# Performance work log

Hardware: AMD Instinct MI355X
Metric: run time of the kernel (lower is better)

The kernel has to match this reference:

```python
import jax, jax.numpy as jnp
import numpy as np
from jax.ops import segment_sum, segment_max

N_NODES = 100000
N_EDGES = 1600000
IN, HID, OUT = 256, 64, 40
NEG_SLOPE = 0.2  # DGL GATConv default


def setup_inputs() -> dict:
    key = jax.random.key(0)
    ks = jax.random.split(key, 12)
    feat = jax.random.normal(ks[0], (N_NODES, IN), dtype=jnp.float32)
    src = jax.random.randint(ks[1], (N_EDGES,), 0, N_NODES)
    dst = jax.random.randint(ks[2], (N_EDGES,), 0, N_NODES)
    def xavier(k, shape):
        fan = sum(shape)
        return jax.random.normal(k, shape, dtype=jnp.float32) * jnp.sqrt(2.0 / fan)
    return {
        "feat": feat, "src": src, "dst": dst,
        "W1": xavier(ks[3], (IN, HID)),  "b1": jnp.zeros((HID,), jnp.float32),
        "al1": xavier(ks[4], (HID,)),    "ar1": xavier(ks[5], (HID,)),
        "W2": xavier(ks[6], (HID, OUT)), "b2": jnp.zeros((OUT,), jnp.float32),
        "al2": xavier(ks[7], (OUT,)),    "ar2": xavier(ks[8], (OUT,)),
    }


def gat_layer(x, W, b, attn_l, attn_r, src, dst, n):
    # z: [N, F_out] projected features
    z = x @ W
    el = z @ attn_l          # [N] source attention logits
    er = z @ attn_r          # [N] destination attention logits
    e = jax.nn.leaky_relu(el[src] + er[dst], NEG_SLOPE)  # [E]
    # segment (per-destination) softmax over incoming edges
    m = segment_max(e, dst, num_segments=n)              # [N]
    w = jnp.exp(e - m[dst])                              # [E]
    s = segment_sum(w, dst, num_segments=n)              # [N]
    alpha = w / s[dst]                                   # [E]
    # scatter-add aggregation of alpha * z[src]
    out = segment_sum(alpha[:, None] * z[src], dst, num_segments=n)
    return out + b


def reference(feat, src, dst, W1, b1, al1, ar1, W2, b2, al2, ar2):
    n = feat.shape[0]
    h = gat_layer(feat, W1, b1, al1, ar1, src, dst, n)
    h = jax.nn.relu(h)  # dropout is identity in eval mode
    h = gat_layer(h, W2, b2, al2, ar2, src, dst, n)
    return jax.nn.log_softmax(h, axis=-1)  # [N, out_size]
```

## Files before the change

### kernel.cpp

```cpp
#include <hip/hip_runtime.h>
#include <math.h>

constexpr int NN   = 100000;
constexpr int NE   = 1600000;
constexpr int FIN  = 256;
constexpr int HID  = 64;
constexpr int FOUT = 40;
constexpr float SLOPE = 0.2f;
constexpr int NBUCK = (NN + 127) / 128;
constexpr int TILE_A = 2048;
constexpr int NWG_A = (NE + TILE_A - 1) / TILE_A;
constexpr int NT_GEMM = (NN + 63) / 64;
constexpr int HB = 64;
constexpr int HIST_EPB = 4096;
constexpr int NWG_H = (NE + HIST_EPB - 1) / HIST_EPB;

typedef short  short8  __attribute__((ext_vector_type(8)));
typedef float  floatx4 __attribute__((ext_vector_type(4)));

__device__ inline unsigned short f2bf(float x) {
    union { float f; unsigned int u; } c; c.f = x;
    unsigned int u = c.u;
    return (unsigned short)((u + 0x7FFF + ((u >> 16) & 1)) >> 16);
}

__device__ inline float readlane_f(float v, int l) {
    return __int_as_float(__builtin_amdgcn_readlane(__float_as_int(v), l));
}

__device__ inline void scan_buckets(const int* __restrict__ gcnt,
                                    int* __restrict__ bofs,
                                    int* __restrict__ tsum, int t)
{
    int i0 = 4 * t;
    int c0 = (i0 + 0 < NBUCK) ? gcnt[i0 + 0] : 0;
    int c1 = (i0 + 1 < NBUCK) ? gcnt[i0 + 1] : 0;
    int c2 = (i0 + 2 < NBUCK) ? gcnt[i0 + 2] : 0;
    int c3 = (i0 + 3 < NBUCK) ? gcnt[i0 + 3] : 0;
    int s = c0 + c1 + c2 + c3;
    tsum[t] = s;
    __syncthreads();
    for (int off = 1; off < 256; off <<= 1) {
        int x = (t >= off) ? tsum[t - off] : 0;
        __syncthreads();
        tsum[t] += x;
        __syncthreads();
    }
    int e0 = tsum[t] - s;
    if (i0 + 0 <= NBUCK) bofs[i0 + 0] = e0;
    if (i0 + 1 <= NBUCK) bofs[i0 + 1] = e0 + c0;
    if (i0 + 2 <= NBUCK) bofs[i0 + 2] = e0 + c0 + c1;
    if (i0 + 3 <= NBUCK) bofs[i0 + 3] = e0 + c0 + c1 + c2;
    __syncthreads();
}

__global__ __launch_bounds__(256) void prep_kernel(
    const float* __restrict__ W1, unsigned short* __restrict__ W1T,
    const float* __restrict__ W2, const float* __restrict__ al2,
    const float* __restrict__ ar2,
    float* __restrict__ wl2, float* __restrict__ wr2,
    const int* __restrict__ dst, int* __restrict__ bcnt)
{
    const int t = threadIdx.x;
    if (blockIdx.x < HB) {
        int idx = blockIdx.x * 256 + t;
        if (idx < FIN * HID) {
            int k = idx >> 6, n = idx & 63;
            W1T[n * FIN + k] = f2bf(W1[idx]);
        }
        if (blockIdx.x == 0 && t < HID) {
            int k = t;
            float a = 0.f, b = 0.f;
            #pragma unroll 8
            for (int j = 0; j < FOUT; ++j) {
                float wv = W2[k * FOUT + j];
                a += wv * al2[j]; b += wv * ar2[j];
            }
            wl2[k] = a; wr2[k] = b;
        }
    } else {
        __shared__ int hist[NBUCK];
        for (int i = t; i < NBUCK; i += 256) hist[i] = 0;
        __syncthreads();
        int base = (blockIdx.x - HB) * HIST_EPB + t * 16;
        #pragma unroll
        for (int k = 0; k < 4; ++k) {
            int idx = base + 4 * k;
            if (idx < NE) {
                const int4 d4 = *(const int4*)&dst[idx];
                atomicAdd(&hist[d4.x >> 7], 1); atomicAdd(&hist[d4.y >> 7], 1);
                atomicAdd(&hist[d4.z >> 7], 1); atomicAdd(&hist[d4.w >> 7], 1);
            }
        }
        __syncthreads();
        for (int i = t; i < NBUCK; i += 256) {
            int hv = hist[i];
            if (hv) atomicAdd(&bcnt[i], hv);
        }
    }
}

__global__ __launch_bounds__(256) void mega_kernel(
    const float* __restrict__ feat, const unsigned short* __restrict__ W1T,
    const float* __restrict__ al, const float* __restrict__ ar,
    const int* __restrict__ src, const int* __restrict__ dst,
    const int* __restrict__ bcnt, int* __restrict__ cur0,
    int* __restrict__ ebuck,
    _Float16* __restrict__ z, float* __restrict__ el, float* __restrict__ er)
{
    __shared__ int smem4[2 * NBUCK + 1 + 256];
    const int t = threadIdx.x;

    if (blockIdx.x < NT_GEMM) {
        const int ntile = blockIdx.x * 64;

        const int w  = t >> 6;
        const int l  = t & 63;
        const int lr = l & 15;
        const int q  = l >> 4;
        const int m0 = 16 * w;

        int n = ntile + m0 + lr; if (n >= NN) n = NN - 1;
        const float* __restrict__ arow = feat + (size_t)n * FIN;

        floatx4 acc[4];
        #pragma unroll
        for (int tile = 0; tile < 4; ++tile) acc[tile] = 0.f;

        #pragma unroll
        for (int kc = 0; kc < 8; ++kc) {
            const int koff = kc * 32 + 8 * q;
            const float4 fa = *(const float4*)(arow + koff);
            const float4 fb = *(const float4*)(arow + koff + 4);
            short8 av;
            av[0] = (short)f2bf(fa.x); av[1] = (short)f2bf(fa.y);
            av[2] = (short)f2bf(fa.z); av[3] = (short)f2bf(fa.w);
            av[4] = (short)f2bf(fb.x); av[5] = (short)f2bf(fb.y);
            av[6] = (short)f2bf(fb.z); av[7] = (short)f2bf(fb.w);
            #pragma unroll
            for (int tile = 0; tile < 4; ++tile) {
                const short8 bv = *(const short8*)(W1T + (16 * tile + lr) * FIN + koff);
                acc[tile] = __builtin_amdgcn_mfma_f32_16x16x32_bf16(av, bv, acc[tile], 0, 0, 0);
            }
        }

        float aln[4], arn[4];
        #pragma unroll
        for (int tile = 0; tile < 4; ++tile) {
            aln[tile] = al[16 * tile + lr];
            arn[tile] = ar[16 * tile + lr];
        }
        #pragma unroll
        for (int r = 0; r < 4; ++r) {
            int mg = ntile + m0 + 4 * q + r;
            float pl = 0.f, pr = 0.f;
            #pragma unroll
            for (int tile = 0; tile < 4; ++tile) {
                float zv = acc[tile][r];
                pl += zv * aln[tile]; pr += zv * arn[tile];
            }
            #pragma unroll
            for (int off = 8; off >= 1; off >>= 1) {
                pl += __shfl_xor(pl, off);
                pr += __shfl_xor(pr, off);
            }
            if (mg < NN) {
                #pragma unroll
                for (int tile = 0; tile < 4; ++tile)
                    z[(size_t)mg * HID + 16 * tile + lr] = (_Float16)acc[tile][r];
                if (lr == 0) { el[mg] = pl; er[mg] = pr; }
            }
        }
    } else {
        int* hist = smem4;
        int* bofs = smem4 + NBUCK;
        int* tsum = smem4 + 2 * NBUCK + 1;
        const int blk = blockIdx.x - NT_GEMM;
        const int e0 = blk * TILE_A;
        const int e1 = (e0 + TILE_A < NE) ? e0 + TILE_A : NE;

        for (int i = t; i < NBUCK; i += 256) hist[i] = 0;
        scan_buckets(bcnt, bofs, tsum, t);
        for (int e = e0 + t; e < e1; e += 256)
            atomicAdd(&hist[dst[e] >> 7], 1);
        __syncthreads();
        for (int i = t; i < NBUCK; i += 256) {
            int hv = hist[i];
            hist[i] = hv ? (bofs[i] + atomicAdd(&cur0[i], hv)) : 0;
        }
        __syncthreads();
        for (int e = e0 + t; e < e1; e += 256) {
            int d = dst[e], s_ = src[e];
            int p = atomicAdd(&hist[d >> 7], 1);
            ebuck[p] = (s_ << 7) | (d & 127);
        }
    }
}

__global__ __launch_bounds__(256) void partB_kernel(
    const int* __restrict__ bcnt, const int* __restrict__ ebuck,
    int* __restrict__ row_ptr, int* __restrict__ esrc)
{
    __shared__ int bofs[NBUCK + 1];
    __shared__ int tsum[256];
    __shared__ int sdeg[128];
    __shared__ int sscan[128];
    __shared__ int scur[128];
    const int b = blockIdx.x;
    const int n0 = b << 7;
    const int t = threadIdx.x;

    if (t < 128) sdeg[t] = 0;
    scan_buckets(bcnt, bofs, tsum, t);
    const int r0 = bofs[b], r1 = bofs[b + 1];

    for (int e = r0 + t; e < r1; e += 256)
        atomicAdd(&sdeg[ebuck[e] & 127], 1);
    __syncthreads();

    if (t < 128) sscan[t] = sdeg[t];
    __syncthreads();
    for (int off = 1; off < 128; off <<= 1) {
        int x = (t < 128 && t >= off) ? sscan[t - off] : 0;
        __syncthreads();
        if (t < 128) sscan[t] += x;
        __syncthreads();
    }
    if (t < 128) {
        int excl = sscan[t] - sdeg[t];
        if (n0 + t < NN) row_ptr[n0 + t] = r0 + excl;
        scur[t] = r0 + excl;
    }
    if (b == NBUCK - 1 && t == 0) row_ptr[NN] = NE;
    __syncthreads();

    for (int e = r0 + t; e < r1; e += 256) {
        int pk = ebuck[e];
        int p = atomicAdd(&scur[pk & 127], 1);
        esrc[p] = pk >> 7;
    }
}

template<bool FIRST>
__global__ __launch_bounds__(256) void gat_gather_kernel(
    const int* __restrict__ row_ptr, const int* __restrict__ esrc,
    const float* __restrict__ el, const float* __restrict__ er,
    const _Float16* __restrict__ zin, const float* __restrict__ b1,
    const float* __restrict__ wl2, const float* __restrict__ wr2,
    _Float16* __restrict__ hout, _Float16* __restrict__ haggout,
    float* __restrict__ el2, float* __restrict__ er2)
{
    const int w = threadIdx.x >> 6, lane = threadIdx.x & 63;
    const int d = blockIdx.x * 4 + w;
    const int r0 = row_ptr[d], r1 = row_ptr[d + 1];
    const int cnt = r1 - r0;
    const float erd = er[d];

    float accv = 0.f;
    float s = 0.f;

    if (cnt <= 64) {
        int sn = 0; float v = -INFINITY;
        if (lane < cnt) {
            sn = esrc[r0 + lane];
            v = el[sn] + erd;
            v = (v >= 0.f) ? v : SLOPE * v;
        }
        float m = v;
        #pragma unroll
        for (int off = 32; off >= 1; off >>= 1) m = fmaxf(m, __shfl_xor(m, off));
        float wv = (lane < cnt) ? __expf(v - m) : 0.f;
        s = wv;
        #pragma unroll
        for (int off = 32; off >= 1; off >>= 1) s += __shfl_xor(s, off);
        {
            int j = 0;
            for (; j + 8 <= cnt; j += 8) {
                float a0 = 0.f, a1 = 0.f;
                #pragma unroll
                for (int qq = 0; qq < 8; qq += 2) {
                    float w0 = readlane_f(wv, j + qq);
                    int   s0 = __builtin_amdgcn_readlane(sn, j + qq);
                    float w1 = readlane_f(wv, j + qq + 1);
                    int   s1 = __builtin_amdgcn_readlane(sn, j + qq + 1);
                    a0 += w0 * (float)zin[(size_t)s0 * HID + lane];
                    a1 += w1 * (float)zin[(size_t)s1 * HID + lane];
                }
                accv += a0 + a1;
            }
            for (; j < cnt; ++j) {
                float w0 = readlane_f(wv, j);
                int   s0 = __builtin_amdgcn_readlane(sn, j);
                accv += w0 * (float)zin[(size_t)s0 * HID + lane];
            }
        }
    } else {
        float m = -INFINITY;
        for (int e = r0 + lane; e < r1; e += 64) {
            float v = el[esrc[e]] + erd;
            v = (v >= 0.f) ? v : SLOPE * v;
            m = fmaxf(m, v);
        }
        #pragma unroll
        for (int off = 32; off >= 1; off >>= 1) m = fmaxf(m, __shfl_xor(m, off));
        for (int base = r0; base < r1; base += 64) {
            int e = base + lane;
            float wv = 0.f; int sn = 0;
            if (e < r1) {
                sn = esrc[e];
                float v = el[sn] + erd;
                v = (v >= 0.f) ? v : SLOPE * v;
                wv = __expf(v - m);
            }
            s += wv;
            int c = r1 - base; if (c > 64) c = 64;
            {
                int j = 0;
                for (; j + 4 <= c; j += 4) {
                    float a0 = 0.f, a1 = 0.f;
                    #pragma unroll
                    for (int qq = 0; qq < 4; qq += 2) {
                        float w0 = readlane_f(wv, j + qq);
                        int   s0 = __builtin_amdgcn_readlane(sn, j + qq);
                        float w1 = readlane_f(wv, j + qq + 1);
                        int   s1 = __builtin_amdgcn_readlane(sn, j + qq + 1);
                        a0 += w0 * (float)zin[(size_t)s0 * HID + lane];
                        a1 += w1 * (float)zin[(size_t)s1 * HID + lane];
                    }
                    accv += a0 + a1;
                }
                for (; j < c; ++j) {
                    float w0 = readlane_f(wv, j);
                    int   s0 = __builtin_amdgcn_readlane(sn, j);
                    accv += w0 * (float)zin[(size_t)s0 * HID + lane];
                }
            }
        }
        #pragma unroll
        for (int off = 32; off >= 1; off >>= 1) s += __shfl_xor(s, off);
    }

    float res = (cnt > 0) ? (accv / s) : 0.f;

    if (FIRST) {
        float hval = res + b1[lane];
        hval = (hval > 0.f) ? hval : 0.f;
        hout[(size_t)d * HID + lane] = (_Float16)hval;
        float pl = hval * wl2[lane];
        float pr = hval * wr2[lane];
        #pragma unroll
        for (int off = 32; off >= 1; off >>= 1) {
            pl += __shfl_xor(pl, off); pr += __shfl_xor(pr, off);
        }
        if (lane == 0) { el2[d] = pl; er2[d] = pr; }
    } else {
        haggout[(size_t)d * HID + lane] = (_Float16)res;
    }
}

__global__ __launch_bounds__(256) void out_kernel(
    const _Float16* __restrict__ hagg, const float* __restrict__ W2,
    const float* __restrict__ b2, float* __restrict__ out)
{
    __shared__ float sh[4][64];
    const int w = threadIdx.x >> 6, lane = threadIdx.x & 63;
    const int n = blockIdx.x * 4 + w;
    sh[w][lane] = (float)hagg[(size_t)n * HID + lane];
    __syncthreads();
    float acc = 0.f;
    if (lane < FOUT) {
        #pragma unroll 8
        for (int k = 0; k < HID; ++k) acc += sh[w][k] * W2[k * FOUT + lane];
    }
    float v = (lane < FOUT) ? acc + b2[lane] : -INFINITY;
    float mx = v;
    #pragma unroll
    for (int off = 32; off >= 1; off >>= 1) mx = fmaxf(mx, __shfl_xor(mx, off));
    float ex = (lane < FOUT) ? __expf(v - mx) : 0.f;
    float sm = ex;
    #pragma unroll
    for (int off = 32; off >= 1; off >>= 1) sm += __shfl_xor(sm, off);
    if (lane < FOUT) out[(size_t)n * FOUT + lane] = v - mx - __logf(sm);
}

extern "C" void kernel_launch(void* const* d_in, const int* in_sizes, int n_in,
                              void* d_out, int out_size, void* d_ws, size_t ws_size,
                              hipStream_t stream) {
    const float* feat = (const float*)d_in[0];
    const int*   src  = (const int*)d_in[1];
    const int*   dst  = (const int*)d_in[2];
    const float* W1   = (const float*)d_in[3];
    const float* b1   = (const float*)d_in[4];
    const float* al1  = (const float*)d_in[5];
    const float* ar1  = (const float*)d_in[6];
    const float* W2   = (const float*)d_in[7];
    const float* b2   = (const float*)d_in[8];
    const float* al2  = (const float*)d_in[9];
    const float* ar2  = (const float*)d_in[10];
    float* out = (float*)d_out;

    char* p = (char*)d_ws;
    _Float16* hagg = (_Float16*)p;
    _Float16* z1   = (_Float16*)p;  p += (size_t)NN * HID * 2;
    _Float16* h    = (_Float16*)p;  p += (size_t)NN * HID * 2;
    float* el1   = (float*)p;     p += (size_t)NN * 4;
    float* er1   = (float*)p;     p += (size_t)NN * 4;
    float* el2   = (float*)p;     p += (size_t)NN * 4;
    float* er2   = (float*)p;     p += (size_t)NN * 4;
    float* wl2   = (float*)p;     p += HID * 4;
    float* wr2   = (float*)p;     p += HID * 4;
    int*   bcnt  = (int*)p;       p += NBUCK * 4;
    int*   cur0  = (int*)p;       p += NBUCK * 4;
    int*   rowp  = (int*)p;       p += (NN + 1) * 4;
    int*   esrc  = (int*)p;       p += (size_t)NE * 4;
    int*   ebuck = (int*)p;       p += (size_t)NE * 4;
    unsigned short* w1t = (unsigned short*)p;

    hipMemsetAsync(bcnt, 0, 2 * NBUCK * sizeof(int), stream);

    prep_kernel<<<HB + NWG_H, 256, 0, stream>>>(
        W1, w1t, W2, al2, ar2, wl2, wr2, dst, bcnt);

    mega_kernel<<<NT_GEMM + NWG_A, 256, 0, stream>>>(
        feat, w1t, al1, ar1, src, dst, bcnt, cur0, ebuck, z1, el1, er1);

    partB_kernel<<<NBUCK, 256, 0, stream>>>(bcnt, ebuck, rowp, esrc);

    gat_gather_kernel<true><<<NN / 4, 256, 0, stream>>>(
        rowp, esrc, el1, er1, z1, b1, wl2, wr2, h, nullptr, el2, er2);

    gat_gather_kernel<false><<<NN / 4, 256, 0, stream>>>(
        rowp, esrc, el2, er2, h, nullptr, nullptr, nullptr,
        nullptr, hagg, nullptr, nullptr);

    out_kernel<<<NN / 4, 256, 0, stream>>>(hagg, W2, b2, out);
}
```

Measured before the change: 435.0 us.

## Fuse pipeline into two cooperative persistent kernels with grid syncs

Replaces the six kernel launches (prep, mega, partB, two gathers, output) with two cooperative persistent kernels. Stages are separated by grid-wide syncs and driven by grid-stride loops. The GEMM stage now stages the transposed bf16 W1 in LDS and takes a fixed 3/4 of the blocks, with the rest doing edge bucketing. The aim is to cut launch and tail overheads between stages, at the cost of grid-sync latency and occupancy-limited grid sizes for the gather phases.

```diff
diff --git a/kernel.cpp b/kernel.cpp
--- a/kernel.cpp
+++ b/kernel.cpp
@@ -1,5 +1,8 @@
 #include <hip/hip_runtime.h>
+#include <hip/hip_cooperative_groups.h>
 #include <math.h>
+
+namespace cg = cooperative_groups;
 
 constexpr int NN   = 100000;
 constexpr int NE   = 1600000;
@@ -9,11 +12,11 @@
 constexpr float SLOPE = 0.2f;
 constexpr int NBUCK = (NN + 127) / 128;
 constexpr int TILE_A = 2048;
-constexpr int NWG_A = (NE + TILE_A - 1) / TILE_A;
+constexpr int PA_CHUNKS = (NE + TILE_A - 1) / TILE_A;
 constexpr int NT_GEMM = (NN + 63) / 64;
-constexpr int HB = 64;
+constexpr int AK = 264;
 constexpr int HIST_EPB = 4096;
-constexpr int NWG_H = (NE + HIST_EPB - 1) / HIST_EPB;
+constexpr int NH = (NE + HIST_EPB - 1) / HIST_EPB;
 
 typedef short  short8  __attribute__((ext_vector_type(8)));
 typedef float  floatx4 __attribute__((ext_vector_type(4)));
@@ -54,65 +57,70 @@
     __syncthreads();
 }
 
-__global__ __launch_bounds__(256) void prep_kernel(
-    const float* __restrict__ W1, unsigned short* __restrict__ W1T,
+__global__ __launch_bounds__(256) void coopA(
+    const float* __restrict__ feat, const float* __restrict__ W1,
+    unsigned short* __restrict__ W1T,
     const float* __restrict__ W2, const float* __restrict__ al2,
     const float* __restrict__ ar2,
     float* __restrict__ wl2, float* __restrict__ wr2,
-    const int* __restrict__ dst, int* __restrict__ bcnt)
+    const int* __restrict__ src, const int* __restrict__ dst,
+    int* __restrict__ bcnt, int* __restrict__ cur0, int* __restrict__ ebuck,
+    const float* __restrict__ al, const float* __restrict__ ar,
+    _Float16* __restrict__ z, float* __restrict__ el, float* __restrict__ er,
+    int* __restrict__ row_ptr, int* __restrict__ esrc)
 {
-    const int t = threadIdx.x;
-    if (blockIdx.x < HB) {
-        int idx = blockIdx.x * 256 + t;
-        if (idx < FIN * HID) {
-            int k = idx >> 6, n = idx & 63;
-            W1T[n * FIN + k] = f2bf(W1[idx]);
-        }
-        if (blockIdx.x == 0 && t < HID) {
-            int k = t;
-            float a = 0.f, b = 0.f;
-            #pragma unroll 8
-            for (int j = 0; j < FOUT; ++j) {
-                float wv = W2[k * FOUT + j];
-                a += wv * al2[j]; b += wv * ar2[j];
-            }
-            wl2[k] = a; wr2[k] = b;
-        }
-    } else {
-        __shared__ int hist[NBUCK];
+    cg::grid_group gridg = cg::this_grid();
+    __shared__ int smem[8448];
+    const int t   = threadIdx.x;
+    const int bid = blockIdx.x;
+    const int G   = gridDim.x;
+
+    for (int idx = bid * 256 + t; idx < FIN * HID; idx += G * 256) {
+        int k = idx >> 6, n = idx & 63;
+        W1T[n * FIN + k] = f2bf(W1[idx]);
+    }
+    if (bid == 0 && t < HID) {
+        float a = 0.f, b = 0.f;
+        #pragma unroll 8
+        for (int j = 0; j < FOUT; ++j) {
+            float wv = W2[t * FOUT + j];
+            a += wv * al2[j]; b += wv * ar2[j];
+        }
+        wl2[t] = a; wr2[t] = b;
+    }
+    for (int hb = bid; hb < NH; hb += G) {
+        int* hist = smem;
         for (int i = t; i < NBUCK; i += 256) hist[i] = 0;
         __syncthreads();
-        int base = (blockIdx.x - HB) * HIST_EPB + t * 16;
-        #pragma unroll
-        for (int k = 0; k < 4; ++k) {
-            int idx = base + 4 * k;
-            if (idx < NE) {
-                const int4 d4 = *(const int4*)&dst[idx];
-                atomicAdd(&hist[d4.x >> 7], 1); atomicAdd(&hist[d4.y >> 7], 1);
-                atomicAdd(&hist[d4.z >> 7], 1); atomicAdd(&hist[d4.w >> 7], 1);
-            }
+        int e0 = hb * HIST_EPB;
+        int e1 = e0 + HIST_EPB; if (e1 > NE) e1 = NE;
+        for (int e = e0 + t * 4; e < e1; e += 1024) {
+            const int4 d4 = *(const int4*)&dst[e];
+            atomicAdd(&hist[d4.x >> 7], 1); atomicAdd(&hist[d4.y >> 7], 1);
+            atomicAdd(&hist[d4.z >> 7], 1); atomicAdd(&hist[d4.w >> 7], 1);
         }
         __syncthreads();
         for (int i = t; i < NBUCK; i += 256) {
             int hv = hist[i];
             if (hv) atomicAdd(&bcnt[i], hv);
         }
-    }
-}
-
-__global__ __launch_bounds__(256) void mega_kernel(
-    const float* __restrict__ feat, const unsigned short* __restrict__ W1T,
-    const float* __restrict__ al, const float* __restrict__ ar,
-    const int* __restrict__ src, const int* __restrict__ dst,
-    const int* __restrict__ bcnt, int* __restrict__ cur0,
-    int* __restrict__ ebuck,
-    _Float16* __restrict__ z, float* __restrict__ el, float* __restrict__ er)
-{
-    __shared__ int smem4[2 * NBUCK + 1 + 256];
-    const int t = threadIdx.x;
-
-    if (blockIdx.x < NT_GEMM) {
-        const int ntile = blockIdx.x * 64;
+        __syncthreads();
+    }
+    gridg.sync();
+
+    int GS = (G * 3) >> 2;
+    if (GS >= G) GS = G - 1;
+    if (GS < 1)  GS = 1;
+
+    if (bid < GS) {
+        unsigned short* sBT = (unsigned short*)smem;
+        #pragma unroll
+        for (int i = 0; i < 8; ++i) {
+            int g2 = t + 256 * i;
+            int row = g2 >> 5, c8 = g2 & 31;
+            *(uint4*)&sBT[row * AK + 8 * c8] = *(const uint4*)&W1T[row * FIN + 8 * c8];
+        }
+        __syncthreads();
 
         const int w  = t >> 6;
         const int l  = t & 63;
@@ -120,130 +128,133 @@
         const int q  = l >> 4;
         const int m0 = 16 * w;
 
-        int n = ntile + m0 + lr; if (n >= NN) n = NN - 1;
-        const float* __restrict__ arow = feat + (size_t)n * FIN;
-
-        floatx4 acc[4];
-        #pragma unroll
-        for (int tile = 0; tile < 4; ++tile) acc[tile] = 0.f;
-
-        #pragma unroll
-        for (int kc = 0; kc < 8; ++kc) {
-            const int koff = kc * 32 + 8 * q;
-            const float4 fa = *(const float4*)(arow + koff);
-            const float4 fb = *(const float4*)(arow + koff + 4);
-            short8 av;
-            av[0] = (short)f2bf(fa.x); av[1] = (short)f2bf(fa.y);
-            av[2] = (short)f2bf(fa.z); av[3] = (short)f2bf(fa.w);
-            av[4] = (short)f2bf(fb.x); av[5] = (short)f2bf(fb.y);
-            av[6] = (short)f2bf(fb.z); av[7] = (short)f2bf(fb.w);
+        float aln[4], arn[4];
+        #pragma unroll
+        for (int ti = 0; ti < 4; ++ti) {
+            aln[ti] = al[16 * ti + lr];
+            arn[ti] = ar[16 * ti + lr];
+        }
+
+        for (int ot = bid; ot < NT_GEMM; ot += GS) {
+            const int ntile = ot * 64;
+            int n = ntile + m0 + lr; if (n >= NN) n = NN - 1;
+            const float* __restrict__ arow = feat + (size_t)n * FIN;
+
+            floatx4 acc[4];
             #pragma unroll
-            for (int tile = 0; tile < 4; ++tile) {
-                const short8 bv = *(const short8*)(W1T + (16 * tile + lr) * FIN + koff);
-                acc[tile] = __builtin_amdgcn_mfma_f32_16x16x32_bf16(av, bv, acc[tile], 0, 0, 0);
-            }
-        }
-
-        float aln[4], arn[4];
-        #pragma unroll
-        for (int tile = 0; tile < 4; ++tile) {
-            aln[tile] = al[16 * tile + lr];
-            arn[tile] = ar[16 * tile + lr];
-        }
-        #pragma unroll
-        for (int r = 0; r < 4; ++r) {
-            int mg = ntile + m0 + 4 * q + r;
-            float pl = 0.f, pr = 0.f;
+            for (int ti = 0; ti < 4; ++ti) acc[ti] = 0.f;
+
             #pragma unroll
-            for (int tile = 0; tile < 4; ++tile) {
-                float zv = acc[tile][r];
-                pl += zv * aln[tile]; pr += zv * arn[tile];
-            }
+            for (int kc = 0; kc < 8; ++kc) {
+                const int koff = kc * 32 + 8 * q;
+                const float4 fa = *(const float4*)(arow + koff);
+                const float4 fb = *(const float4*)(arow + koff + 4);
+                short8 av;
+                av[0] = (short)f2bf(fa.x); av[1] = (short)f2bf(fa.y);
+                av[2] = (short)f2bf(fa.z); av[3] = (short)f2bf(fa.w);
+                av[4] = (short)f2bf(fb.x); av[5] = (short)f2bf(fb.y);
+                av[6] = (short)f2bf(fb.z); av[7] = (short)f2bf(fb.w);
+                #pragma unroll
+                for (int ti = 0; ti < 4; ++ti) {
+                    const short8 bv = *(const short8*)(sBT + (16 * ti + lr) * AK + koff);
+                    acc[ti] = __builtin_amdgcn_mfma_f32_16x16x32_bf16(av, bv, acc[ti], 0, 0, 0);
+                }
+            }
+
             #pragma unroll
-            for (int off = 8; off >= 1; off >>= 1) {
-                pl += __shfl_xor(pl, off);
-                pr += __shfl_xor(pr, off);
-            }
-            if (mg < NN) {
+            for (int r = 0; r < 4; ++r) {
+                int mg = ntile + m0 + 4 * q + r;
+                float pl = 0.f, pr = 0.f;
                 #pragma unroll
-                for (int tile = 0; tile < 4; ++tile)
-                    z[(size_t)mg * HID + 16 * tile + lr] = (_Float16)acc[tile][r];
-                if (lr == 0) { el[mg] = pl; er[mg] = pr; }
+                for (int ti = 0; ti < 4; ++ti) {
+                    float zv = acc[ti][r];
+                    pl += zv * aln[ti]; pr += zv * arn[ti];
+                }
+                #pragma unroll
+                for (int off = 8; off >= 1; off >>= 1) {
+                    pl += __shfl_xor(pl, off);
+                    pr += __shfl_xor(pr, off);
+                }
+                if (mg < NN) {
+                    #pragma unroll
+                    for (int ti = 0; ti < 4; ++ti)
+                        z[(size_t)mg * HID + 16 * ti + lr] = (_Float16)acc[ti][r];
+                    if (lr == 0) { el[mg] = pl; er[mg] = pr; }
+                }
             }
         }
     } else {
-        int* hist = smem4;
-        int* bofs = smem4 + NBUCK;
-        int* tsum = smem4 + 2 * NBUCK + 1;
-        const int blk = blockIdx.x - NT_GEMM;
-        const int e0 = blk * TILE_A;
-        const int e1 = (e0 + TILE_A < NE) ? e0 + TILE_A : NE;
-
-        for (int i = t; i < NBUCK; i += 256) hist[i] = 0;
+        int* hist = smem;
+        int* bofs = smem + NBUCK;
+        int* tsum = smem + 2 * NBUCK + 1;
         scan_buckets(bcnt, bofs, tsum, t);
-        for (int e = e0 + t; e < e1; e += 256)
-            atomicAdd(&hist[dst[e] >> 7], 1);
-        __syncthreads();
-        for (int i = t; i < NBUCK; i += 256) {
-            int hv = hist[i];
-            hist[i] = hv ? (bofs[i] + atomicAdd(&cur0[i], hv)) : 0;
-        }
-        __syncthreads();
-        for (int e = e0 + t; e < e1; e += 256) {
-            int d = dst[e], s_ = src[e];
-            int p = atomicAdd(&hist[d >> 7], 1);
-            ebuck[p] = (s_ << 7) | (d & 127);
-        }
-    }
-}
-
-__global__ __launch_bounds__(256) void partB_kernel(
-    const int* __restrict__ bcnt, const int* __restrict__ ebuck,
-    int* __restrict__ row_ptr, int* __restrict__ esrc)
-{
-    __shared__ int bofs[NBUCK + 1];
-    __shared__ int tsum[256];
-    __shared__ int sdeg[128];
-    __shared__ int sscan[128];
-    __shared__ int scur[128];
-    const int b = blockIdx.x;
-    const int n0 = b << 7;
-    const int t = threadIdx.x;
-
-    if (t < 128) sdeg[t] = 0;
-    scan_buckets(bcnt, bofs, tsum, t);
-    const int r0 = bofs[b], r1 = bofs[b + 1];
-
-    for (int e = r0 + t; e < r1; e += 256)
-        atomicAdd(&sdeg[ebuck[e] & 127], 1);
-    __syncthreads();
-
-    if (t < 128) sscan[t] = sdeg[t];
-    __syncthreads();
-    for (int off = 1; off < 128; off <<= 1) {
-        int x = (t < 128 && t >= off) ? sscan[t - off] : 0;
-        __syncthreads();
-        if (t < 128) sscan[t] += x;
-        __syncthreads();
-    }
-    if (t < 128) {
-        int excl = sscan[t] - sdeg[t];
-        if (n0 + t < NN) row_ptr[n0 + t] = r0 + excl;
-        scur[t] = r0 + excl;
-    }
-    if (b == NBUCK - 1 && t == 0) row_ptr[NN] = NE;
-    __syncthreads();
-
-    for (int e = r0 + t; e < r1; e += 256) {
-        int pk = ebuck[e];
-        int p = atomicAdd(&scur[pk & 127], 1);
-        esrc[p] = pk >> 7;
+        const int NPA = G - GS;
+        for (int c = bid - GS; c < PA_CHUNKS; c += NPA) {
+            const int e0 = c * TILE_A;
+            int e1 = e0 + TILE_A; if (e1 > NE) e1 = NE;
+            for (int i = t; i < NBUCK; i += 256) hist[i] = 0;
+            __syncthreads();
+            for (int e = e0 + t; e < e1; e += 256)
+                atomicAdd(&hist[dst[e] >> 7], 1);
+            __syncthreads();
+            for (int i = t; i < NBUCK; i += 256) {
+                int hv = hist[i];
+                hist[i] = hv ? (bofs[i] + atomicAdd(&cur0[i], hv)) : 0;
+            }
+            __syncthreads();
+            for (int e = e0 + t; e < e1; e += 256) {
+                int d = dst[e], s_ = src[e];
+                int p = atomicAdd(&hist[d >> 7], 1);
+                ebuck[p] = (s_ << 7) | (d & 127);
+            }
+            __syncthreads();
+        }
+    }
+    gridg.sync();
+
+    {
+        int* sdeg  = smem;
+        int* sscan = smem + 128;
+        int* scur  = smem + 256;
+        int* bofs  = smem + 384;
+        int* tsum  = smem + 384 + NBUCK + 1;
+        scan_buckets(bcnt, bofs, tsum, t);
+        for (int b = bid; b < NBUCK; b += G) {
+            const int n0 = b << 7;
+            if (t < 128) sdeg[t] = 0;
+            __syncthreads();
+            const int r0 = bofs[b], r1 = bofs[b + 1];
+            for (int e = r0 + t; e < r1; e += 256)
+                atomicAdd(&sdeg[ebuck[e] & 127], 1);
+            __syncthreads();
+            if (t < 128) sscan[t] = sdeg[t];
+            __syncthreads();
+            for (int off = 1; off < 128; off <<= 1) {
+                int x = (t < 128 && t >= off) ? sscan[t - off] : 0;
+                __syncthreads();
+                if (t < 128) sscan[t] += x;
+                __syncthreads();
+            }
+            if (t < 128) {
+                int excl = sscan[t] - sdeg[t];
+                if (n0 + t < NN) row_ptr[n0 + t] = r0 + excl;
+                scur[t] = r0 + excl;
+            }
+            if (b == NBUCK - 1 && t == 0) row_ptr[NN] = NE;
+            __syncthreads();
+            for (int e = r0 + t; e < r1; e += 256) {
+                int pk = ebuck[e];
+                int p = atomicAdd(&scur[pk & 127], 1);
+                esrc[p] = pk >> 7;
+            }
+            __syncthreads();
+        }
     }
 }
 
 template<bool FIRST>
-__global__ __launch_bounds__(256) void gat_gather_kernel(
-    const int* __restrict__ row_ptr, const int* __restrict__ esrc,
+__device__ inline void gather_blk(
+    int blk, const int* __restrict__ row_ptr, const int* __restrict__ esrc,
     const float* __restrict__ el, const float* __restrict__ er,
     const _Float16* __restrict__ zin, const float* __restrict__ b1,
     const float* __restrict__ wl2, const float* __restrict__ wr2,
@@ -251,7 +262,7 @@
     float* __restrict__ el2, float* __restrict__ er2)
 {
     const int w = threadIdx.x >> 6, lane = threadIdx.x & 63;
-    const int d = blockIdx.x * 4 + w;
+    const int d = blk * 4 + w;
     const int r0 = row_ptr[d], r1 = row_ptr[d + 1];
     const int cnt = r1 - r0;
     const float erd = er[d];
@@ -358,29 +369,49 @@
     }
 }
 
-__global__ __launch_bounds__(256) void out_kernel(
-    const _Float16* __restrict__ hagg, const float* __restrict__ W2,
-    const float* __restrict__ b2, float* __restrict__ out)
+__global__ __launch_bounds__(256) void coopB(
+    const int* __restrict__ row_ptr, const int* __restrict__ esrc,
+    const float* __restrict__ el1, const float* __restrict__ er1,
+    const _Float16* __restrict__ z1, const float* __restrict__ b1,
+    const float* __restrict__ wl2, const float* __restrict__ wr2,
+    _Float16* __restrict__ h, float* __restrict__ el2, float* __restrict__ er2,
+    _Float16* __restrict__ hagg,
+    const float* __restrict__ W2, const float* __restrict__ b2,
+    float* __restrict__ out)
 {
+    cg::grid_group gridg = cg::this_grid();
     __shared__ float sh[4][64];
+    const int G = gridDim.x;
+
+    for (int blk = blockIdx.x; blk < NN / 4; blk += G)
+        gather_blk<true>(blk, row_ptr, esrc, el1, er1, z1, b1, wl2, wr2,
+                         h, nullptr, el2, er2);
+    gridg.sync();
+
+    for (int blk = blockIdx.x; blk < NN / 4; blk += G)
+        gather_blk<false>(blk, row_ptr, esrc, el2, er2, h, nullptr, nullptr,
+                          nullptr, nullptr, hagg, nullptr, nullptr);
+    gridg.sync();
+
     const int w = threadIdx.x >> 6, lane = threadIdx.x & 63;
-    const int n = blockIdx.x * 4 + w;
-    sh[w][lane] = (float)hagg[(size_t)n * HID + lane];
-    __syncthreads();
-    float acc = 0.f;
-    if (lane < FOUT) {
-        #pragma unroll 8
-        for (int k = 0; k < HID; ++k) acc += sh[w][k] * W2[k * FOUT + lane];
-    }
-    float v = (lane < FOUT) ? acc + b2[lane] : -INFINITY;
-    float mx = v;
-    #pragma unroll
-    for (int off = 32; off >= 1; off >>= 1) mx = fmaxf(mx, __shfl_xor(mx, off));
-    float ex = (lane < FOUT) ? __expf(v - mx) : 0.f;
-    float sm = ex;
-    #pragma unroll
-    for (int off = 32; off >= 1; off >>= 1) sm += __shfl_xor(sm, off);
-    if (lane < FOUT) out[(size_t)n * FOUT + lane] = v - mx - __logf(sm);
+    for (int blk = blockIdx.x; blk < NN / 4; blk += G) {
+        const int n = blk * 4 + w;
+        sh[w][lane] = (float)hagg[(size_t)n * HID + lane];
+        float acc = 0.f;
+        if (lane < FOUT) {
+            #pragma unroll 8
+            for (int k = 0; k < HID; ++k) acc += sh[w][k] * W2[k * FOUT + lane];
+        }
+        float v = (lane < FOUT) ? acc + b2[lane] : -INFINITY;
+        float mx = v;
+        #pragma unroll
+        for (int off = 32; off >= 1; off >>= 1) mx = fmaxf(mx, __shfl_xor(mx, off));
+        float ex = (lane < FOUT) ? __expf(v - mx) : 0.f;
+        float sm = ex;
+        #pragma unroll
+        for (int off = 32; off >= 1; off >>= 1) sm += __shfl_xor(sm, off);
+        if (lane < FOUT) out[(size_t)n * FOUT + lane] = v - mx - __logf(sm);
+    }
 }
 
 extern "C" void kernel_launch(void* const* d_in, const int* in_sizes, int n_in,
@@ -416,22 +447,34 @@
     int*   ebuck = (int*)p;       p += (size_t)NE * 4;
     unsigned short* w1t = (unsigned short*)p;
 
+    static int gA = 0, gB = 0;
+    if (gA == 0) {
+        int dev = 0; hipGetDevice(&dev);
+        hipDeviceProp_t prop; hipGetDeviceProperties(&prop, dev);
+        int bA = 0, bB = 0;
+        hipOccupancyMaxActiveBlocksPerMultiprocessor(&bA, coopA, 256, 0);
+        hipOccupancyMaxActiveBlocksPerMultiprocessor(&bB, coopB, 256, 0);
+        if (bA < 1) bA = 1;
+        if (bB < 1) bB = 1;
+        gA = bA * prop.multiProcessorCount;
+        gB = bB * prop.multiProcessorCount;
+        if (gA > 2048) gA = 2048;
+        if (gB > 2048) gB = 2048;
+        if (gA < 2) gA = 2;
+    }
+
     hipMemsetAsync(bcnt, 0, 2 * NBUCK * sizeof(int), stream);
 
-    prep_kernel<<<HB + NWG_H, 256, 0, stream>>>(
-        W1, w1t, W2, al2, ar2, wl2, wr2, dst, bcnt);
-
-    mega_kernel<<<NT_GEMM + NWG_A, 256, 0, stream>>>(
-        feat, w1t, al1, ar1, src, dst, bcnt, cur0, ebuck, z1, el1, er1);
-
-    partB_kernel<<<NBUCK, 256, 0, stream>>>(bcnt, ebuck, rowp, esrc);
-
-    gat_gather_kernel<true><<<NN / 4, 256, 0, stream>>>(
-        rowp, esrc, el1, er1, z1, b1, wl2, wr2, h, nullptr, el2, er2);
-
-    gat_gather_kernel<false><<<NN / 4, 256, 0, stream>>>(
-        rowp, esrc, el2, er2, h, nullptr, nullptr, nullptr,
-        nullptr, hagg, nullptr, nullptr);
-
-    out_kernel<<<NN / 4, 256, 0, stream>>>(hagg, W2, b2, out);
-}
+    void* argsA[] = {
+        (void*)&feat, (void*)&W1, (void*)&w1t, (void*)&W2, (void*)&al2,
+        (void*)&ar2, (void*)&wl2, (void*)&wr2, (void*)&src, (void*)&dst,
+        (void*)&bcnt, (void*)&cur0, (void*)&ebuck, (void*)&al1, (void*)&ar1,
+        (void*)&z1, (void*)&el1, (void*)&er1, (void*)&rowp, (void*)&esrc };
+    hipLaunchCooperativeKernel(coopA, dim3(gA), dim3(256), argsA, 0, stream);
+
+    void* argsB[] = {
+        (void*)&rowp, (void*)&esrc, (void*)&el1, (void*)&er1, (void*)&z1,
+        (void*)&b1, (void*)&wl2, (void*)&wr2, (void*)&h, (void*)&el2,
+        (void*)&er2, (void*)&hagg, (void*)&W2, (void*)&b2, (void*)&out };
+    hipLaunchCooperativeKernel(coopB, dim3(gB), dim3(256), argsB, 0, stream);
+}
```

After: 857.8 us. 1.97x slower.

## Stage W1 in swizzled LDS for GEMM and batch gather loads in aggregation

Applied to the files above, without the earlier changes.

The GEMM blocks of the fused kernel now copy the bf16 W1 transpose into shared memory with an XOR swizzle, then read the MFMA B operand from LDS instead of global memory. The bucket-scatter path moves its cursor array into a separate region of the enlarged shared buffer. The aggregation loops now issue 16 independent feature gathers before accumulating, raising memory-level parallelism. The cost is a 32KB LDS allocation per block, which may reduce occupancy for the edge-bucketing blocks, plus higher register pressure in the aggregation kernel.

```diff
diff --git a/kernel.cpp b/kernel.cpp
--- a/kernel.cpp
+++ b/kernel.cpp
@@ -108,11 +108,21 @@
     int* __restrict__ ebuck,
     _Float16* __restrict__ z, float* __restrict__ el, float* __restrict__ er)
 {
-    __shared__ int smem4[2 * NBUCK + 1 + 256];
+    __shared__ int smem4[8192];
     const int t = threadIdx.x;
 
     if (blockIdx.x < NT_GEMM) {
+        char* sBT = (char*)smem4;
         const int ntile = blockIdx.x * 64;
+
+        #pragma unroll
+        for (int i = 0; i < 8; ++i) {
+            int g = t + 256 * i;
+            int row = g >> 5, c8 = g & 31;
+            int off16 = (c8 << 4) ^ ((row & 7) << 4);
+            *(uint4*)(sBT + row * 512 + off16) = *(const uint4*)&W1T[row * FIN + 8 * c8];
+        }
+        __syncthreads();
 
         const int w  = t >> 6;
         const int l  = t & 63;
@@ -139,7 +149,9 @@
             av[6] = (short)f2bf(fb.z); av[7] = (short)f2bf(fb.w);
             #pragma unroll
             for (int tile = 0; tile < 4; ++tile) {
-                const short8 bv = *(const short8*)(W1T + (16 * tile + lr) * FIN + koff);
+                const int row = 16 * tile + lr;
+                const int byt = row * 512 + ((koff * 2) ^ ((row & 7) << 4));
+                const short8 bv = *(const short8*)(sBT + byt);
                 acc[tile] = __builtin_amdgcn_mfma_f32_16x16x32_bf16(av, bv, acc[tile], 0, 0, 0);
             }
         }
@@ -175,6 +187,7 @@
         int* hist = smem4;
         int* bofs = smem4 + NBUCK;
         int* tsum = smem4 + 2 * NBUCK + 1;
+        int* lcur = smem4 + 2 * NBUCK + 1 + 256;
         const int blk = blockIdx.x - NT_GEMM;
         const int e0 = blk * TILE_A;
         const int e1 = (e0 + TILE_A < NE) ? e0 + TILE_A : NE;
@@ -186,12 +199,12 @@
         __syncthreads();
         for (int i = t; i < NBUCK; i += 256) {
             int hv = hist[i];
-            hist[i] = hv ? (bofs[i] + atomicAdd(&cur0[i], hv)) : 0;
+            lcur[i] = hv ? (bofs[i] + atomicAdd(&cur0[i], hv)) : 0;
         }
         __syncthreads();
         for (int e = e0 + t; e < e1; e += 256) {
             int d = dst[e], s_ = src[e];
-            int p = atomicAdd(&hist[d >> 7], 1);
+            int p = atomicAdd(&lcur[d >> 7], 1);
             ebuck[p] = (s_ << 7) | (d & 127);
         }
     }
@@ -275,18 +288,27 @@
         for (int off = 32; off >= 1; off >>= 1) s += __shfl_xor(s, off);
         {
             int j = 0;
-            for (; j + 8 <= cnt; j += 8) {
-                float a0 = 0.f, a1 = 0.f;
+            for (; j + 16 <= cnt; j += 16) {
+                float wb[16], zb[16];
                 #pragma unroll
-                for (int qq = 0; qq < 8; qq += 2) {
-                    float w0 = readlane_f(wv, j + qq);
-                    int   s0 = __builtin_amdgcn_readlane(sn, j + qq);
-                    float w1 = readlane_f(wv, j + qq + 1);
-                    int   s1 = __builtin_amdgcn_readlane(sn, j + qq + 1);
-                    a0 += w0 * (float)zin[(size_t)s0 * HID + lane];
-                    a1 += w1 * (float)zin[(size_t)s1 * HID + lane];
+                for (int u = 0; u < 16; ++u) {
+                    wb[u] = readlane_f(wv, j + u);
+                    int su = __builtin_amdgcn_readlane(sn, j + u);
+                    zb[u] = (float)zin[(size_t)su * HID + lane];
                 }
-                accv += a0 + a1;
+                #pragma unroll
+                for (int u = 0; u < 16; ++u) accv += wb[u] * zb[u];
+            }
+            for (; j + 4 <= cnt; j += 4) {
+                float wb[4], zb[4];
+                #pragma unroll
+                for (int u = 0; u < 4; ++u) {
+                    wb[u] = readlane_f(wv, j + u);
+                    int su = __builtin_amdgcn_readlane(sn, j + u);
+                    zb[u] = (float)zin[(size_t)su * HID + lane];
+                }
+                #pragma unroll
+                for (int u = 0; u < 4; ++u) accv += wb[u] * zb[u];
             }
             for (; j < cnt; ++j) {
                 float w0 = readlane_f(wv, j);
@@ -316,18 +338,16 @@
             int c = r1 - base; if (c > 64) c = 64;
             {
                 int j = 0;
-                for (; j + 4 <= c; j += 4) {
-                    float a0 = 0.f, a1 = 0.f;
+                for (; j + 16 <= c; j += 16) {
+                    float wb[16], zb[16];
                     #pragma unroll
-                    for (int qq = 0; qq < 4; qq += 2) {
-                        float w0 = readlane_f(wv, j + qq);
-                        int   s0 = __builtin_amdgcn_readlane(sn, j + qq);
-                        float w1 = readlane_f(wv, j + qq + 1);
-                        int   s1 = __builtin_amdgcn_readlane(sn, j + qq + 1);
-                        a0 += w0 * (float)zin[(size_t)s0 * HID + lane];
-                        a1 += w1 * (float)zin[(size_t)s1 * HID + lane];
+                    for (int u = 0; u < 16; ++u) {
+                        wb[u] = readlane_f(wv, j + u);
+                        int su = __builtin_amdgcn_readlane(sn, j + u);
+                        zb[u] = (float)zin[(size_t)su * HID + lane];
                     }
-                    accv += a0 + a1;
+                    #pragma unroll
+                    for (int u = 0; u < 16; ++u) accv += wb[u] * zb[u];
                 }
                 for (; j < c; ++j) {
                     float w0 = readlane_f(wv, j);
```

After: 422.9 us. 1.03x faster.
